# Performance work log

Hardware: AMD Instinct MI355X
Metric: run time of the kernel (lower is better)

## Reference

```python
import jax, jax.numpy as jnp
import numpy as np

K = 128
HEADS = 8

def setup_inputs() -> dict:
    key = jax.random.key(0)
    ks = jax.random.split(key, 6)
    B, S = 4, 2048
    x = jax.random.normal(ks[0], (B, S, K), dtype=jnp.float32)
    sc = 1.0 / np.sqrt(K)
    Wq = jax.random.normal(ks[1], (K, K * HEADS), dtype=jnp.float32) * sc
    Wk = jax.random.normal(ks[2], (K, K * HEADS), dtype=jnp.float32) * sc
    Wv = jax.random.normal(ks[3], (K, K * HEADS), dtype=jnp.float32) * sc
    Wo = jax.random.normal(ks[4], (HEADS * K, K), dtype=jnp.float32) * (1.0 / np.sqrt(HEADS * K))
    bo = jnp.zeros((K,), dtype=jnp.float32)
    return {"x": x, "Wq": Wq, "Wk": Wk, "Wv": Wv, "Wo": Wo, "bo": bo}

def reference(x, Wq, Wk, Wv, Wo, bo):
    B, S, k = x.shape
    h = HEADS
    # projections: (B,S,k) @ (k, k*h) -> (B,S,h,k) -> (B,h,S,k)
    q = (x @ Wq).reshape(B, S, h, k).transpose(0, 2, 1, 3)
    kk = (x @ Wk).reshape(B, S, h, k).transpose(0, 2, 1, 3)
    v = (x @ Wv).reshape(B, S, h, k).transpose(0, 2, 1, 3)
    scale = k ** -0.25
    q = q * scale
    kk = kk * scale
    scores = jnp.einsum('bhqd,bhkd->bhqk', q, kk)  # (B,h,S,S)
    attn = jax.nn.softmax(scores, axis=-1)
    out = jnp.einsum('bhqk,bhkd->bhqd', attn, v)  # (B,h,S,k)
    out = out.transpose(0, 2, 1, 3).reshape(B, S, h * k)
    return out @ Wo + bo
```

## Files before the change

### kernel.cpp

```cpp
#include <hip/hip_runtime.h>


typedef __attribute__((ext_vector_type(8))) short bf16x8;
typedef __attribute__((ext_vector_type(4))) float f32x4;
typedef __attribute__((ext_vector_type(16))) float f32x16;
typedef __attribute__((ext_vector_type(4))) int i32x4;

#define LOG2E 1.4426950408889634f

__device__ __forceinline__ unsigned short f2bf(float f) {
  unsigned u = __builtin_bit_cast(unsigned, f);
  return (unsigned short)((u + 0x7fffu + ((u >> 16) & 1u)) >> 16);
}

__device__ __forceinline__ unsigned cvtpk(float lo, float hi) {
  unsigned r;
  asm("v_cvt_pk_bf16_f32 %0, %1, %2" : "=v"(r) : "v"(lo), "v"(hi));
  return r;
}

__global__ void prep_kernel(const float* __restrict__ x, const float* __restrict__ Wq,
                            const float* __restrict__ Wk, const float* __restrict__ Wv,
                            const float* __restrict__ Wo,
                            unsigned short* __restrict__ xb, unsigned short* __restrict__ Wtq,
                            unsigned short* __restrict__ Wtk, unsigned short* __restrict__ Wtv,
                            unsigned short* __restrict__ Wot) {
  int tid = blockIdx.x * 256 + threadIdx.x;
  if (tid < 8192 * 128) xb[tid] = f2bf(x[tid]);
  if (tid < 1024 * 128) {
    int r = tid >> 7, c = tid & 127;
    Wtq[tid] = f2bf(Wq[c * 1024 + r]);
    Wtk[tid] = f2bf(Wk[c * 1024 + r]);
    Wtv[tid] = f2bf(Wv[c * 1024 + r]);
    int r2 = tid >> 10, c2 = tid & 1023;
    Wot[tid] = f2bf(Wo[c2 * 128 + r2]);
  }
}

__device__ __forceinline__ void stage_64x128(unsigned short* dst, const unsigned short* gsrc, int t) {
#pragma unroll
  for (int it = 0; it < 4; ++it) {
    int c = t + it * 256;
    int row = c >> 4, col = c & 15;
    *(f32x4*)((char*)dst + row * 256 + ((col * 16) ^ ((row & 7) << 4))) =
        *(const f32x4*)(gsrc + row * 128 + col * 8);
  }
}

__device__ __forceinline__ void mfma_64x64(const unsigned short* As, const unsigned short* Bs,
                                           int w, int l, f32x4 acc[4]) {
  int lc = l & 15, kg = l >> 4;
#pragma unroll
  for (int kc = 0; kc < 4; ++kc) {
    int ar = w * 16 + lc;
    bf16x8 a = *(const bf16x8*)((const char*)As + ar * 256 + ((kc * 64 + kg * 16) ^ ((ar & 7) << 4)));
#pragma unroll
    for (int tt = 0; tt < 4; ++tt) {
      int br = tt * 16 + lc;
      bf16x8 b = *(const bf16x8*)((const char*)Bs + br * 256 + ((kc * 64 + kg * 16) ^ ((br & 7) << 4)));
      acc[tt] = __builtin_amdgcn_mfma_f32_16x16x32_bf16(a, b, acc[tt], 0, 0, 0);
    }
  }
}

__global__ __launch_bounds__(256) void proj_qk_kernel(const unsigned short* __restrict__ xb,
    const unsigned short* __restrict__ Wtq, const unsigned short* __restrict__ Wtk,
    unsigned short* __restrict__ Qb, unsigned short* __restrict__ Kb) {
  __shared__ unsigned short As[64 * 128], Bs[64 * 128];
  const unsigned short* Wt = blockIdx.z ? Wtk : Wtq;
  unsigned short* Out = blockIdx.z ? Kb : Qb;
  int m0 = blockIdx.x * 64, n0 = blockIdx.y * 64;
  int t = threadIdx.x, w = t >> 6, l = t & 63, lc = l & 15, kg = l >> 4;
  stage_64x128(As, xb + m0 * 128, t);
  stage_64x128(Bs, Wt + n0 * 128, t);
  __syncthreads();
  f32x4 acc[4];
#pragma unroll
  for (int i = 0; i < 4; ++i) acc[i] = (f32x4){0.f, 0.f, 0.f, 0.f};
  mfma_64x64(As, Bs, w, l, acc);
  const float scale = 0.29730177875068026f;
#pragma unroll
  for (int tt = 0; tt < 4; ++tt)
#pragma unroll
    for (int e = 0; e < 4; ++e) {
      int m = m0 + w * 16 + kg * 4 + e;
      int n = n0 + tt * 16 + lc;
      int b = m >> 11, s = m & 2047, h = n >> 7, d = n & 127;
      Out[((b * 8 + h) * 2048 + s) * 128 + d] = f2bf(acc[tt][e] * scale);
    }
}

__global__ __launch_bounds__(256) void proj_v_kernel(const unsigned short* __restrict__ xb,
    const unsigned short* __restrict__ Wtv, unsigned short* __restrict__ Vt) {
  __shared__ unsigned short As[64 * 128], Bs[64 * 128];
  int n0 = blockIdx.x * 64;
  int t0 = blockIdx.y * 64;
  int t = threadIdx.x, w = t >> 6, l = t & 63, lc = l & 15, kg = l >> 4;
  stage_64x128(As, Wtv + n0 * 128, t);
  stage_64x128(Bs, xb + t0 * 128, t);
  __syncthreads();
  f32x4 acc[4];
#pragma unroll
  for (int i = 0; i < 4; ++i) acc[i] = (f32x4){0.f, 0.f, 0.f, 0.f};
  mfma_64x64(As, Bs, w, l, acc);
#pragma unroll
  for (int tt = 0; tt < 4; ++tt)
#pragma unroll
    for (int e = 0; e < 4; ++e) {
      int n = n0 + w * 16 + kg * 4 + e;
      int m = t0 + tt * 16 + lc;
      int b = m >> 11, s = m & 2047, h = n >> 7, d = n & 127;
      Vt[((b * 8 + h) * 128 + d) * 2048 + s] = f2bf(acc[tt][e]);
    }
}

__global__ __launch_bounds__(256, 2) void attn_kernel(const unsigned short* __restrict__ Qb,
    const unsigned short* __restrict__ Kb, const unsigned short* __restrict__ Vt,
    unsigned short* __restrict__ att) {
  __shared__ unsigned short lds[2][16384];
  int bid = blockIdx.x;
  int fid = (bid & 7) * 64 + (bid >> 3);
  int bh = fid >> 4, qt = fid & 15;
  const unsigned short* Qp = Qb + bh * 2048 * 128;
  const unsigned short* Kp = Kb + bh * 2048 * 128;
  const unsigned short* Vp = Vt + bh * 128 * 2048;
  int t = threadIdx.x, w = t >> 6, l = t & 63, lc = l & 31, hi = l >> 5;
  int q0 = qt * 128 + w * 32;

  bf16x8 qf[8];
  {
    const unsigned short* qr_ = Qp + (q0 + lc) * 128 + hi * 8;
#pragma unroll
    for (int kc = 0; kc < 8; ++kc) qf[kc] = *(const bf16x8*)(qr_ + kc * 16);
  }

  int kcol = l & 15, vc = l & 7;
  int krow[4], vrow[4];
#pragma unroll
  for (int i = 0; i < 4; ++i) { krow[i] = w * 16 + i * 4 + (l >> 4); vrow[i] = w * 32 + i * 8 + (l >> 3); }

  f32x16 acc[4];
#pragma unroll
  for (int i = 0; i < 4; ++i)
#pragma unroll
    for (int j = 0; j < 16; ++j) acc[i][j] = 0.f;
  float m_run = -1e30f, l_run = 0.f;

  f32x4 sk[4], sv[4];
#pragma unroll
  for (int i = 0; i < 4; ++i) {
    sk[i] = *(const f32x4*)(Kp + krow[i] * 128 + kcol * 8);
    sv[i] = *(const f32x4*)(Vp + vrow[i] * 2048 + vc * 8);
  }
#pragma unroll
  for (int i = 0; i < 4; ++i) {
    *(f32x4*)((char*)&lds[0][0] + krow[i] * 256 + ((kcol * 16) ^ ((krow[i] & 7) << 4))) = sk[i];
    *(f32x4*)((char*)&lds[0][8192] + vrow[i] * 128 + ((vc * 16) ^ ((vrow[i] & 7) << 4))) = sv[i];
  }
  __syncthreads();

  for (int kt = 0; kt < 32; ++kt) {
    int cur = kt & 1;
    if (kt < 31) {
      int kv0 = (kt + 1) * 64;
#pragma unroll
      for (int i = 0; i < 4; ++i) {
        sk[i] = *(const f32x4*)(Kp + (kv0 + krow[i]) * 128 + kcol * 8);
        sv[i] = *(const f32x4*)(Vp + vrow[i] * 2048 + kv0 + vc * 8);
      }
    }
    const char* Kb_ = (const char*)&lds[cur][0];
    const char* Vb_ = (const char*)&lds[cur][8192];

    f32x16 s0, s1;
#pragma unroll
    for (int j = 0; j < 16; ++j) { s0[j] = 0.f; s1[j] = 0.f; }
#pragma unroll
    for (int kc = 0; kc < 8; ++kc) {
      int cb = kc * 32 + hi * 16;
      int r1 = 32 + lc;
      bf16x8 k0 = *(const bf16x8*)(Kb_ + lc * 256 + (cb ^ ((lc & 7) << 4)));
      bf16x8 k1 = *(const bf16x8*)(Kb_ + r1 * 256 + (cb ^ ((r1 & 7) << 4)));
      s0 = __builtin_amdgcn_mfma_f32_32x32x16_bf16(k0, qf[kc], s0, 0, 0, 0);
      s1 = __builtin_amdgcn_mfma_f32_32x32x16_bf16(k1, qf[kc], s1, 0, 0, 0);
    }

    float pmax = s0[0];
#pragma unroll
    for (int j = 1; j < 16; ++j) pmax = fmaxf(pmax, s0[j]);
#pragma unroll
    for (int j = 0; j < 16; ++j) pmax = fmaxf(pmax, s1[j]);
    pmax = fmaxf(pmax, __shfl_xor(pmax, 32));
    float mold = m_run;
    bool defer = __all(pmax <= m_run + 8.f) != 0;
    if (!defer) m_run = fmaxf(m_run, pmax);
    float rs = 0.f;
#pragma unroll
    for (int j = 0; j < 16; ++j) { s0[j] = __builtin_exp2f((s0[j] - m_run) * LOG2E); rs += s0[j]; }
#pragma unroll
    for (int j = 0; j < 16; ++j) { s1[j] = __builtin_exp2f((s1[j] - m_run) * LOG2E); rs += s1[j]; }
    rs += __shfl_xor(rs, 32);
    if (!defer) {
      float resc = __builtin_exp2f((mold - m_run) * LOG2E);
      l_run = l_run * resc + rs;
#pragma unroll
      for (int r = 0; r < 16; ++r) {
        int qr = (r & 3) + 8 * (r >> 2) + 4 * hi;
        float f = __shfl(resc, qr, 32);
#pragma unroll
        for (int dt = 0; dt < 4; ++dt) acc[dt][r] *= f;
      }
    } else {
      l_run += rs;
    }

    bf16x8 pa[4];
#define PACK(ks, SX, o) { \
      unsigned a1 = cvtpk(SX[o], SX[(o) + 1]); \
      unsigned b1 = cvtpk(SX[(o) + 4], SX[(o) + 5]); \
      unsigned a2 = cvtpk(SX[(o) + 2], SX[(o) + 3]); \
      unsigned b2 = cvtpk(SX[(o) + 6], SX[(o) + 7]); \
      unsigned pa1 = (unsigned)__shfl_xor((int)a1, 32), pb1 = (unsigned)__shfl_xor((int)b1, 32); \
      unsigned pa2 = (unsigned)__shfl_xor((int)a2, 32), pb2 = (unsigned)__shfl_xor((int)b2, 32); \
      i32x4 pp; \
      pp[0] = (int)(hi ? pb1 : a1); pp[1] = (int)(hi ? pb2 : a2); \
      pp[2] = (int)(hi ? b1 : pa1); pp[3] = (int)(hi ? b2 : pa2); \
      pa[ks] = __builtin_bit_cast(bf16x8, pp); }
    PACK(0, s0, 0) PACK(1, s0, 8) PACK(2, s1, 0) PACK(3, s1, 8)
#undef PACK

#pragma unroll
    for (int ks = 0; ks < 4; ++ks) {
      int cb = ks * 32 + hi * 16;
#pragma unroll
      for (int dt = 0; dt < 4; ++dt) {
        int vr = dt * 32 + lc;
        bf16x8 vb = *(const bf16x8*)(Vb_ + vr * 128 + (cb ^ ((vr & 7) << 4)));
        acc[dt] = __builtin_amdgcn_mfma_f32_32x32x16_bf16(pa[ks], vb, acc[dt], 0, 0, 0);
      }
    }

    if (kt < 31) {
      char* Kn = (char*)&lds[cur ^ 1][0];
      char* Vn = (char*)&lds[cur ^ 1][8192];
#pragma unroll
      for (int i = 0; i < 4; ++i) {
        *(f32x4*)(Kn + krow[i] * 256 + ((kcol * 16) ^ ((krow[i] & 7) << 4))) = sk[i];
        *(f32x4*)(Vn + vrow[i] * 128 + ((vc * 16) ^ ((vrow[i] & 7) << 4))) = sv[i];
      }
    }
    __syncthreads();
  }

  int b = bh >> 3, h = bh & 7;
#pragma unroll
  for (int r = 0; r < 16; ++r) {
    int qr = (r & 3) + 8 * (r >> 2) + 4 * hi;
    float linv = 1.f / __shfl(l_run, qr, 32);
    unsigned short* orow = att + ((b * 2048 + (q0 + qr)) * 8 + h) * 128 + lc;
#pragma unroll
    for (int dt = 0; dt < 4; ++dt) orow[dt * 32] = f2bf(acc[dt][r] * linv);
  }
}

__global__ __launch_bounds__(256) void out_proj_kernel(const unsigned short* __restrict__ att,
    const unsigned short* __restrict__ Wot, const float* __restrict__ bo,
    float* __restrict__ out) {
  __shared__ unsigned short As[64 * 128], Bs[64 * 128];
  int m0 = blockIdx.x * 64, n0 = blockIdx.y * 64;
  int t = threadIdx.x, w = t >> 6, l = t & 63, lc = l & 15, kg = l >> 4;
  f32x4 acc[4];
#pragma unroll
  for (int i = 0; i < 4; ++i) acc[i] = (f32x4){0.f, 0.f, 0.f, 0.f};
  for (int kt = 0; kt < 8; ++kt) {
    if (kt) __syncthreads();
#pragma unroll
    for (int it = 0; it < 4; ++it) {
      int c = t + it * 256;
      int row = c >> 4, col = c & 15;
      *(f32x4*)((char*)As + row * 256 + ((col * 16) ^ ((row & 7) << 4))) =
          *(const f32x4*)(att + (m0 + row) * 1024 + kt * 128 + col * 8);
      *(f32x4*)((char*)Bs + row * 256 + ((col * 16) ^ ((row & 7) << 4))) =
          *(const f32x4*)(Wot + (n0 + row) * 1024 + kt * 128 + col * 8);
    }
    __syncthreads();
    mfma_64x64(As, Bs, w, l, acc);
  }
#pragma unroll
  for (int tt = 0; tt < 4; ++tt)
#pragma unroll
    for (int e = 0; e < 4; ++e) {
      int m = m0 + w * 16 + kg * 4 + e;
      int n = n0 + tt * 16 + lc;
      out[m * 128 + n] = acc[tt][e] + bo[n];
    }
}

extern "C" void kernel_launch(void* const* d_in, const int* in_sizes, int n_in,
                              void* d_out, int out_size, void* d_ws, size_t ws_size,
                              hipStream_t stream) {
  const float* x  = (const float*)d_in[0];
  const float* Wq = (const float*)d_in[1];
  const float* Wk = (const float*)d_in[2];
  const float* Wv = (const float*)d_in[3];
  const float* Wo = (const float*)d_in[4];
  const float* bo = (const float*)d_in[5];
  float* out = (float*)d_out;
  char* ws = (char*)d_ws;
  unsigned short* xb  = (unsigned short*)(ws);
  unsigned short* Wtq = (unsigned short*)(ws + (2u << 20));
  unsigned short* Wtk = (unsigned short*)(ws + (2u << 20) + (256u << 10));
  unsigned short* Wtv = (unsigned short*)(ws + (2u << 20) + (512u << 10));
  unsigned short* Wot = (unsigned short*)(ws + (2u << 20) + (768u << 10));
  unsigned short* Qb  = (unsigned short*)(ws + (3u << 20));
  unsigned short* Kb  = (unsigned short*)(ws + (3u << 20) + (16u << 20));
  unsigned short* Vt  = (unsigned short*)(ws + (3u << 20) + (32u << 20));
  unsigned short* att = (unsigned short*)(ws + (3u << 20) + (48u << 20));

  hipLaunchKernelGGL(prep_kernel, dim3(4096), dim3(256), 0, stream,
                     x, Wq, Wk, Wv, Wo, xb, Wtq, Wtk, Wtv, Wot);
  hipLaunchKernelGGL(proj_qk_kernel, dim3(128, 16, 2), dim3(256), 0, stream,
                     xb, Wtq, Wtk, Qb, Kb);
  hipLaunchKernelGGL(proj_v_kernel, dim3(16, 128), dim3(256), 0, stream,
                     xb, Wtv, Vt);
  hipLaunchKernelGGL(attn_kernel, dim3(512), dim3(256), 0, stream,
                     Qb, Kb, Vt, att);
  hipLaunchKernelGGL(out_proj_kernel, dim3(128, 2), dim3(256), 0, stream,
                     att, Wot, bo, out);
}
```

Baseline: 197.2 us.

## Fuse QKV projections into one tiled kernel and streamline attention softmax

Merges the separate Q/K and V projection kernels into one 128x128-tile kernel. That kernel reuses the staged x tile across all three weight matrices and prefetches the next weight tile into registers. In attention, log2e is folded into the Q scale so the raw v_exp_f32 can be used, the max and sum reductions become trees, and lane exchange uses v_permlane32_swap in place of shuffles. It also raises wave priority around the MFMA sections and widens the defer threshold to match the log2 domain. The out-projection now prefetches its next K-slice into registers, which costs register pressure and risks occupancy.

```diff
diff --git a/kernel.cpp b/kernel.cpp
--- a/kernel.cpp
+++ b/kernel.cpp
@@ -16,6 +16,12 @@
 __device__ __forceinline__ unsigned cvtpk(float lo, float hi) {
   unsigned r;
   asm("v_cvt_pk_bf16_f32 %0, %1, %2" : "=v"(r) : "v"(lo), "v"(hi));
+  return r;
+}
+
+__device__ __forceinline__ float vexp2(float x) {
+  float r;
+  asm("v_exp_f32 %0, %1" : "=v"(r) : "v"(x));
   return r;
 }
 
@@ -37,81 +43,131 @@
   }
 }
 
-__device__ __forceinline__ void stage_64x128(unsigned short* dst, const unsigned short* gsrc, int t) {
-#pragma unroll
-  for (int it = 0; it < 4; ++it) {
-    int c = t + it * 256;
-    int row = c >> 4, col = c & 15;
+__device__ __forceinline__ void prefetch8(f32x4* r, const unsigned short* gsrc, int t) {
+#pragma unroll
+  for (int it = 0; it < 8; ++it) {
+    int c = t + it * 256, row = c >> 4, col = c & 15;
+    r[it] = *(const f32x4*)(gsrc + row * 128 + col * 8);
+  }
+}
+
+__device__ __forceinline__ void write8(unsigned short* dst, const f32x4* r, int t) {
+#pragma unroll
+  for (int it = 0; it < 8; ++it) {
+    int c = t + it * 256, row = c >> 4, col = c & 15;
+    *(f32x4*)((char*)dst + row * 256 + ((col * 16) ^ ((row & 7) << 4))) = r[it];
+  }
+}
+
+__device__ __forceinline__ void stage_128x128(unsigned short* dst, const unsigned short* gsrc, int t) {
+#pragma unroll
+  for (int it = 0; it < 8; ++it) {
+    int c = t + it * 256, row = c >> 4, col = c & 15;
     *(f32x4*)((char*)dst + row * 256 + ((col * 16) ^ ((row & 7) << 4))) =
         *(const f32x4*)(gsrc + row * 128 + col * 8);
   }
 }
 
-__device__ __forceinline__ void mfma_64x64(const unsigned short* As, const unsigned short* Bs,
-                                           int w, int l, f32x4 acc[4]) {
+__device__ __forceinline__ void mma128(const unsigned short* As, const unsigned short* Bs,
+                                       int wm, int wn, int l, f32x4 acc[4][4]) {
   int lc = l & 15, kg = l >> 4;
 #pragma unroll
   for (int kc = 0; kc < 4; ++kc) {
-    int ar = w * 16 + lc;
-    bf16x8 a = *(const bf16x8*)((const char*)As + ar * 256 + ((kc * 64 + kg * 16) ^ ((ar & 7) << 4)));
-#pragma unroll
-    for (int tt = 0; tt < 4; ++tt) {
-      int br = tt * 16 + lc;
-      bf16x8 b = *(const bf16x8*)((const char*)Bs + br * 256 + ((kc * 64 + kg * 16) ^ ((br & 7) << 4)));
-      acc[tt] = __builtin_amdgcn_mfma_f32_16x16x32_bf16(a, b, acc[tt], 0, 0, 0);
-    }
-  }
-}
-
-__global__ __launch_bounds__(256) void proj_qk_kernel(const unsigned short* __restrict__ xb,
+    bf16x8 a[4], b[4];
+#pragma unroll
+    for (int mi = 0; mi < 4; ++mi) {
+      int ar = wm * 64 + mi * 16 + lc;
+      a[mi] = *(const bf16x8*)((const char*)As + ar * 256 + ((kc * 64 + kg * 16) ^ ((ar & 7) << 4)));
+    }
+#pragma unroll
+    for (int ni = 0; ni < 4; ++ni) {
+      int br = wn * 64 + ni * 16 + lc;
+      b[ni] = *(const bf16x8*)((const char*)Bs + br * 256 + ((kc * 64 + kg * 16) ^ ((br & 7) << 4)));
+    }
+#pragma unroll
+    for (int mi = 0; mi < 4; ++mi)
+#pragma unroll
+      for (int ni = 0; ni < 4; ++ni)
+        acc[mi][ni] = __builtin_amdgcn_mfma_f32_16x16x32_bf16(a[mi], b[ni], acc[mi][ni], 0, 0, 0);
+  }
+}
+
+__global__ __launch_bounds__(256, 2) void qkv_kernel(const unsigned short* __restrict__ xb,
     const unsigned short* __restrict__ Wtq, const unsigned short* __restrict__ Wtk,
-    unsigned short* __restrict__ Qb, unsigned short* __restrict__ Kb) {
-  __shared__ unsigned short As[64 * 128], Bs[64 * 128];
-  const unsigned short* Wt = blockIdx.z ? Wtk : Wtq;
-  unsigned short* Out = blockIdx.z ? Kb : Qb;
-  int m0 = blockIdx.x * 64, n0 = blockIdx.y * 64;
-  int t = threadIdx.x, w = t >> 6, l = t & 63, lc = l & 15, kg = l >> 4;
-  stage_64x128(As, xb + m0 * 128, t);
-  stage_64x128(Bs, Wt + n0 * 128, t);
-  __syncthreads();
-  f32x4 acc[4];
-#pragma unroll
-  for (int i = 0; i < 4; ++i) acc[i] = (f32x4){0.f, 0.f, 0.f, 0.f};
-  mfma_64x64(As, Bs, w, l, acc);
-  const float scale = 0.29730177875068026f;
-#pragma unroll
-  for (int tt = 0; tt < 4; ++tt)
-#pragma unroll
-    for (int e = 0; e < 4; ++e) {
-      int m = m0 + w * 16 + kg * 4 + e;
-      int n = n0 + tt * 16 + lc;
-      int b = m >> 11, s = m & 2047, h = n >> 7, d = n & 127;
-      Out[((b * 8 + h) * 2048 + s) * 128 + d] = f2bf(acc[tt][e] * scale);
-    }
-}
-
-__global__ __launch_bounds__(256) void proj_v_kernel(const unsigned short* __restrict__ xb,
-    const unsigned short* __restrict__ Wtv, unsigned short* __restrict__ Vt) {
-  __shared__ unsigned short As[64 * 128], Bs[64 * 128];
-  int n0 = blockIdx.x * 64;
-  int t0 = blockIdx.y * 64;
-  int t = threadIdx.x, w = t >> 6, l = t & 63, lc = l & 15, kg = l >> 4;
-  stage_64x128(As, Wtv + n0 * 128, t);
-  stage_64x128(Bs, xb + t0 * 128, t);
-  __syncthreads();
-  f32x4 acc[4];
-#pragma unroll
-  for (int i = 0; i < 4; ++i) acc[i] = (f32x4){0.f, 0.f, 0.f, 0.f};
-  mfma_64x64(As, Bs, w, l, acc);
-#pragma unroll
-  for (int tt = 0; tt < 4; ++tt)
-#pragma unroll
-    for (int e = 0; e < 4; ++e) {
-      int n = n0 + w * 16 + kg * 4 + e;
-      int m = t0 + tt * 16 + lc;
-      int b = m >> 11, s = m & 2047, h = n >> 7, d = n & 127;
-      Vt[((b * 8 + h) * 128 + d) * 2048 + s] = f2bf(acc[tt][e]);
-    }
+    const unsigned short* __restrict__ Wtv,
+    unsigned short* __restrict__ Qb, unsigned short* __restrict__ Kb,
+    unsigned short* __restrict__ Vt) {
+  __shared__ unsigned short Xs[128 * 128], Ws[128 * 128];
+  int m0 = blockIdx.x * 128, n0 = blockIdx.y * 128;
+  int t = threadIdx.x, w = t >> 6, l = t & 63;
+  int wm = w & 1, wn = w >> 1, lc = l & 15, kg = l >> 4;
+  stage_128x128(Xs, xb + m0 * 128, t);
+  stage_128x128(Ws, Wtq + n0 * 128, t);
+  __syncthreads();
+
+  f32x4 rw[8];
+  prefetch8(rw, Wtk + n0 * 128, t);
+
+  f32x4 acc[4][4];
+#pragma unroll
+  for (int mi = 0; mi < 4; ++mi)
+#pragma unroll
+    for (int ni = 0; ni < 4; ++ni) acc[mi][ni] = (f32x4){0.f, 0.f, 0.f, 0.f};
+  mma128(Xs, Ws, wm, wn, l, acc);
+  const float qscale = 0.29730177875068026f * LOG2E;
+#pragma unroll
+  for (int mi = 0; mi < 4; ++mi)
+#pragma unroll
+    for (int ni = 0; ni < 4; ++ni)
+#pragma unroll
+      for (int e = 0; e < 4; ++e) {
+        int m = m0 + wm * 64 + mi * 16 + kg * 4 + e;
+        int n = n0 + wn * 64 + ni * 16 + lc;
+        int b = m >> 11, s = m & 2047, h = n >> 7, d = n & 127;
+        Qb[((b * 8 + h) * 2048 + s) * 128 + d] = f2bf(acc[mi][ni][e] * qscale);
+      }
+  __syncthreads();
+  write8(Ws, rw, t);
+  __syncthreads();
+  prefetch8(rw, Wtv + n0 * 128, t);
+
+#pragma unroll
+  for (int mi = 0; mi < 4; ++mi)
+#pragma unroll
+    for (int ni = 0; ni < 4; ++ni) acc[mi][ni] = (f32x4){0.f, 0.f, 0.f, 0.f};
+  mma128(Xs, Ws, wm, wn, l, acc);
+  const float kscale = 0.29730177875068026f;
+#pragma unroll
+  for (int mi = 0; mi < 4; ++mi)
+#pragma unroll
+    for (int ni = 0; ni < 4; ++ni)
+#pragma unroll
+      for (int e = 0; e < 4; ++e) {
+        int m = m0 + wm * 64 + mi * 16 + kg * 4 + e;
+        int n = n0 + wn * 64 + ni * 16 + lc;
+        int b = m >> 11, s = m & 2047, h = n >> 7, d = n & 127;
+        Kb[((b * 8 + h) * 2048 + s) * 128 + d] = f2bf(acc[mi][ni][e] * kscale);
+      }
+  __syncthreads();
+  write8(Ws, rw, t);
+  __syncthreads();
+
+#pragma unroll
+  for (int mi = 0; mi < 4; ++mi)
+#pragma unroll
+    for (int ni = 0; ni < 4; ++ni) acc[mi][ni] = (f32x4){0.f, 0.f, 0.f, 0.f};
+  mma128(Ws, Xs, wm, wn, l, acc);
+#pragma unroll
+  for (int mi = 0; mi < 4; ++mi)
+#pragma unroll
+    for (int ni = 0; ni < 4; ++ni)
+#pragma unroll
+      for (int e = 0; e < 4; ++e) {
+        int n = n0 + wm * 64 + mi * 16 + kg * 4 + e;
+        int m = m0 + wn * 64 + ni * 16 + lc;
+        int b = m >> 11, s = m & 2047, h = n >> 7, d = n & 127;
+        Vt[((b * 8 + h) * 128 + d) * 2048 + s] = f2bf(acc[mi][ni][e]);
+      }
 }
 
 __global__ __launch_bounds__(256, 2) void attn_kernel(const unsigned short* __restrict__ Qb,
@@ -175,6 +231,7 @@
     f32x16 s0, s1;
 #pragma unroll
     for (int j = 0; j < 16; ++j) { s0[j] = 0.f; s1[j] = 0.f; }
+    __builtin_amdgcn_s_setprio(1);
 #pragma unroll
     for (int kc = 0; kc < 8; ++kc) {
       int cb = kc * 32 + hi * 16;
@@ -184,24 +241,30 @@
       s0 = __builtin_amdgcn_mfma_f32_32x32x16_bf16(k0, qf[kc], s0, 0, 0, 0);
       s1 = __builtin_amdgcn_mfma_f32_32x32x16_bf16(k1, qf[kc], s1, 0, 0, 0);
     }
-
-    float pmax = s0[0];
-#pragma unroll
-    for (int j = 1; j < 16; ++j) pmax = fmaxf(pmax, s0[j]);
-#pragma unroll
-    for (int j = 0; j < 16; ++j) pmax = fmaxf(pmax, s1[j]);
+    __builtin_amdgcn_s_setprio(0);
+
+    float t8[8];
+#pragma unroll
+    for (int j = 0; j < 8; ++j)
+      t8[j] = fmaxf(fmaxf(s0[j], s0[j + 8]), fmaxf(s1[j], s1[j + 8]));
+    float pmax = fmaxf(fmaxf(fmaxf(t8[0], t8[1]), fmaxf(t8[2], t8[3])),
+                       fmaxf(fmaxf(t8[4], t8[5]), fmaxf(t8[6], t8[7])));
     pmax = fmaxf(pmax, __shfl_xor(pmax, 32));
     float mold = m_run;
-    bool defer = __all(pmax <= m_run + 8.f) != 0;
+    bool defer = (__all(pmax <= m_run + 11.5416f) != 0);
     if (!defer) m_run = fmaxf(m_run, pmax);
-    float rs = 0.f;
-#pragma unroll
-    for (int j = 0; j < 16; ++j) { s0[j] = __builtin_exp2f((s0[j] - m_run) * LOG2E); rs += s0[j]; }
-#pragma unroll
-    for (int j = 0; j < 16; ++j) { s1[j] = __builtin_exp2f((s1[j] - m_run) * LOG2E); rs += s1[j]; }
+#pragma unroll
+    for (int j = 0; j < 16; ++j) s0[j] = vexp2(s0[j] - m_run);
+#pragma unroll
+    for (int j = 0; j < 16; ++j) s1[j] = vexp2(s1[j] - m_run);
+    float q8[8];
+#pragma unroll
+    for (int j = 0; j < 8; ++j)
+      q8[j] = (s0[j] + s0[j + 8]) + (s1[j] + s1[j + 8]);
+    float rs = ((q8[0] + q8[1]) + (q8[2] + q8[3])) + ((q8[4] + q8[5]) + (q8[6] + q8[7]));
     rs += __shfl_xor(rs, 32);
     if (!defer) {
-      float resc = __builtin_exp2f((mold - m_run) * LOG2E);
+      float resc = vexp2(mold - m_run);
       l_run = l_run * resc + rs;
 #pragma unroll
       for (int r = 0; r < 16; ++r) {
@@ -216,19 +279,19 @@
 
     bf16x8 pa[4];
 #define PACK(ks, SX, o) { \
-      unsigned a1 = cvtpk(SX[o], SX[(o) + 1]); \
-      unsigned b1 = cvtpk(SX[(o) + 4], SX[(o) + 5]); \
-      unsigned a2 = cvtpk(SX[(o) + 2], SX[(o) + 3]); \
-      unsigned b2 = cvtpk(SX[(o) + 6], SX[(o) + 7]); \
-      unsigned pa1 = (unsigned)__shfl_xor((int)a1, 32), pb1 = (unsigned)__shfl_xor((int)b1, 32); \
-      unsigned pa2 = (unsigned)__shfl_xor((int)a2, 32), pb2 = (unsigned)__shfl_xor((int)b2, 32); \
+      unsigned x1 = cvtpk(SX[o], SX[(o) + 1]); \
+      unsigned y1 = cvtpk(SX[(o) + 4], SX[(o) + 5]); \
+      unsigned x2 = cvtpk(SX[(o) + 2], SX[(o) + 3]); \
+      unsigned y2 = cvtpk(SX[(o) + 6], SX[(o) + 7]); \
+      asm("v_permlane32_swap_b32 %0, %1" : "+v"(x1), "+v"(y1)); \
+      asm("v_permlane32_swap_b32 %0, %1" : "+v"(x2), "+v"(y2)); \
       i32x4 pp; \
-      pp[0] = (int)(hi ? pb1 : a1); pp[1] = (int)(hi ? pb2 : a2); \
-      pp[2] = (int)(hi ? b1 : pa1); pp[3] = (int)(hi ? b2 : pa2); \
+      pp[0] = (int)x1; pp[1] = (int)x2; pp[2] = (int)y1; pp[3] = (int)y2; \
       pa[ks] = __builtin_bit_cast(bf16x8, pp); }
     PACK(0, s0, 0) PACK(1, s0, 8) PACK(2, s1, 0) PACK(3, s1, 8)
 #undef PACK
 
+    __builtin_amdgcn_s_setprio(1);
 #pragma unroll
     for (int ks = 0; ks < 4; ++ks) {
       int cb = ks * 32 + hi * 16;
@@ -239,6 +302,7 @@
         acc[dt] = __builtin_amdgcn_mfma_f32_32x32x16_bf16(pa[ks], vb, acc[dt], 0, 0, 0);
       }
     }
+    __builtin_amdgcn_s_setprio(0);
 
     if (kt < 31) {
       char* Kn = (char*)&lds[cur ^ 1][0];
@@ -260,6 +324,22 @@
     unsigned short* orow = att + ((b * 2048 + (q0 + qr)) * 8 + h) * 128 + lc;
 #pragma unroll
     for (int dt = 0; dt < 4; ++dt) orow[dt * 32] = f2bf(acc[dt][r] * linv);
+  }
+}
+
+__device__ __forceinline__ void mfma_64x64(const unsigned short* As, const unsigned short* Bs,
+                                           int w, int l, f32x4 acc[4]) {
+  int lc = l & 15, kg = l >> 4;
+#pragma unroll
+  for (int kc = 0; kc < 4; ++kc) {
+    int ar = w * 16 + lc;
+    bf16x8 a = *(const bf16x8*)((const char*)As + ar * 256 + ((kc * 64 + kg * 16) ^ ((ar & 7) << 4)));
+#pragma unroll
+    for (int tt = 0; tt < 4; ++tt) {
+      int br = tt * 16 + lc;
+      bf16x8 b = *(const bf16x8*)((const char*)Bs + br * 256 + ((kc * 64 + kg * 16) ^ ((br & 7) << 4)));
+      acc[tt] = __builtin_amdgcn_mfma_f32_16x16x32_bf16(a, b, acc[tt], 0, 0, 0);
+    }
   }
 }
 
@@ -272,18 +352,30 @@
   f32x4 acc[4];
 #pragma unroll
   for (int i = 0; i < 4; ++i) acc[i] = (f32x4){0.f, 0.f, 0.f, 0.f};
+  f32x4 ra[4], rb[4];
+#pragma unroll
+  for (int it = 0; it < 4; ++it) {
+    int c = t + it * 256, row = c >> 4, col = c & 15;
+    ra[it] = *(const f32x4*)(att + (m0 + row) * 1024 + col * 8);
+    rb[it] = *(const f32x4*)(Wot + (n0 + row) * 1024 + col * 8);
+  }
   for (int kt = 0; kt < 8; ++kt) {
     if (kt) __syncthreads();
 #pragma unroll
     for (int it = 0; it < 4; ++it) {
-      int c = t + it * 256;
-      int row = c >> 4, col = c & 15;
-      *(f32x4*)((char*)As + row * 256 + ((col * 16) ^ ((row & 7) << 4))) =
-          *(const f32x4*)(att + (m0 + row) * 1024 + kt * 128 + col * 8);
-      *(f32x4*)((char*)Bs + row * 256 + ((col * 16) ^ ((row & 7) << 4))) =
-          *(const f32x4*)(Wot + (n0 + row) * 1024 + kt * 128 + col * 8);
+      int c = t + it * 256, row = c >> 4, col = c & 15;
+      *(f32x4*)((char*)As + row * 256 + ((col * 16) ^ ((row & 7) << 4))) = ra[it];
+      *(f32x4*)((char*)Bs + row * 256 + ((col * 16) ^ ((row & 7) << 4))) = rb[it];
     }
     __syncthreads();
+    if (kt < 7) {
+#pragma unroll
+      for (int it = 0; it < 4; ++it) {
+        int c = t + it * 256, row = c >> 4, col = c & 15;
+        ra[it] = *(const f32x4*)(att + (m0 + row) * 1024 + (kt + 1) * 128 + col * 8);
+        rb[it] = *(const f32x4*)(Wot + (n0 + row) * 1024 + (kt + 1) * 128 + col * 8);
+      }
+    }
     mfma_64x64(As, Bs, w, l, acc);
   }
 #pragma unroll
@@ -319,10 +411,8 @@
 
   hipLaunchKernelGGL(prep_kernel, dim3(4096), dim3(256), 0, stream,
                      x, Wq, Wk, Wv, Wo, xb, Wtq, Wtk, Wtv, Wot);
-  hipLaunchKernelGGL(proj_qk_kernel, dim3(128, 16, 2), dim3(256), 0, stream,
-                     xb, Wtq, Wtk, Qb, Kb);
-  hipLaunchKernelGGL(proj_v_kernel, dim3(16, 128), dim3(256), 0, stream,
-                     xb, Wtv, Vt);
+  hipLaunchKernelGGL(qkv_kernel, dim3(64, 8), dim3(256), 0, stream,
+                     xb, Wtq, Wtk, Wtv, Qb, Kb, Vt);
   hipLaunchKernelGGL(attn_kernel, dim3(512), dim3(256), 0, stream,
                      Qb, Kb, Vt, att);
   hipLaunchKernelGGL(out_proj_kernel, dim3(128, 2), dim3(256), 0, stream,
```

Result: faster. 175.8 us (-10.8%).
